# Optimization experiments

Measured on AMD Instinct MI355X. Metric: run time of the kernel, lower is better.

The kernel has to match this reference:

```python
import jax, jax.numpy as jnp
import numpy as np

N = 50000
E = 800000
IN_CH = 128
HID = 16
HEADS = 8
OUT_CH = 64
NEG_SLOPE = 0.2


def setup_inputs() -> dict:
    key = jax.random.key(0)
    ks = jax.random.split(key, 16)
    x = jax.random.normal(ks[0], (N, IN_CH), dtype=jnp.float32)
    edge_index = jax.random.randint(ks[1], (2, E), 0, N, dtype=jnp.int64)
    s = 0.05
    # GATv2 layer 1: in=128 -> heads=8, out=16 (concat -> 128)
    W1l = jax.random.normal(ks[2], (IN_CH, HEADS * HID), dtype=jnp.float32) * s
    b1l = jnp.zeros((HEADS * HID,), dtype=jnp.float32)
    W1r = jax.random.normal(ks[3], (IN_CH, HEADS * HID), dtype=jnp.float32) * s
    b1r = jnp.zeros((HEADS * HID,), dtype=jnp.float32)
    att1 = jax.random.normal(ks[4], (HEADS, HID), dtype=jnp.float32) * s
    bias1 = jnp.zeros((HEADS * HID,), dtype=jnp.float32)
    # GATv2 layer 2: in=128 -> heads=1, out=64
    W2l = jax.random.normal(ks[5], (HEADS * HID, OUT_CH), dtype=jnp.float32) * s
    b2l = jnp.zeros((OUT_CH,), dtype=jnp.float32)
    W2r = jax.random.normal(ks[6], (HEADS * HID, OUT_CH), dtype=jnp.float32) * s
    b2r = jnp.zeros((OUT_CH,), dtype=jnp.float32)
    att2 = jax.random.normal(ks[7], (1, OUT_CH), dtype=jnp.float32) * s
    bias2 = jnp.zeros((OUT_CH,), dtype=jnp.float32)
    return dict(x=x, edge_index=edge_index,
                W1l=W1l, b1l=b1l, W1r=W1r, b1r=b1r, att1=att1, bias1=bias1,
                W2l=W2l, b2l=b2l, W2r=W2r, b2r=b2r, att2=att2, bias2=bias2)


def gatv2_conv(x, src, dst, Wl, bl, Wr, br, att, bias, heads, out_ch, concat):
    n = x.shape[0]
    xl = (x @ Wl + bl).reshape(n, heads, out_ch)  # source transform
    xr = (x @ Wr + br).reshape(n, heads, out_ch)  # target transform
    m = xl[src] + xr[dst]                          # [E, H, C]
    m = jnp.where(m > 0, m, NEG_SLOPE * m)         # LeakyReLU(0.2)
    alpha = jnp.einsum('ehc,hc->eh', m, att)       # [E, H]
    # segment softmax over destination nodes (every node has a self loop)
    amax = jax.ops.segment_max(alpha, dst, num_segments=n)
    ea = jnp.exp(alpha - amax[dst])
    denom = jax.ops.segment_sum(ea, dst, num_segments=n)
    w = ea / denom[dst]                            # [E, H]
    out = jax.ops.segment_sum(xl[src] * w[:, :, None], dst, num_segments=n)
    if concat:
        out = out.reshape(n, heads * out_ch)
    else:
        out = out.mean(axis=1)
    return out + bias


def reference(x, edge_index, W1l, b1l, W1r, b1r, att1, bias1,
              W2l, b2l, W2r, b2r, att2, bias2):
    n = x.shape[0]
    loops = jnp.arange(n, dtype=edge_index.dtype)
    src = jnp.concatenate([edge_index[0], loops])
    dst = jnp.concatenate([edge_index[1], loops])
    # dropout layers are identity in eval mode
    h = gatv2_conv(x, src, dst, W1l, b1l, W1r, b1r, att1, bias1,
                   heads=HEADS, out_ch=HID, concat=True)
    h = jax.nn.elu(h)
    out = gatv2_conv(h, src, dst, W2l, b2l, W2r, b2r, att2, bias2,
                     heads=1, out_ch=OUT_CH, concat=True)
    return out
```

## Files before the change

### kernel.cpp

```cpp
#include <hip/hip_runtime.h>
#include <hip/hip_bf16.h>

constexpr int N_  = 50000;
constexpr int E_  = 800000;
constexpr int ET_ = 850000;
constexpr float NEG_SLOPE = 0.2f;

constexpr int CAP  = 48;
constexpr int HT   = ET_ / 8;
constexpr int SB   = (HT + 255) / 256;
constexpr int G1B  = N_ / 16;
constexpr int ZERO4 = (N_ * CAP + N_) / 4;

typedef __attribute__((ext_vector_type(8))) short short8;
typedef __attribute__((ext_vector_type(4))) float f32x4;

__device__ inline unsigned bf16rn(float f) {
    union { float f; unsigned u; } v; v.f = f;
    return (v.u + 0x7fffu + ((v.u >> 16) & 1u)) >> 16;
}
__device__ inline float2 unpack2(unsigned u) {
    return make_float2(__uint_as_float(u << 16), __uint_as_float(u & 0xffff0000u));
}

__global__ __launch_bounds__(256) void init_kernel(
        const float* __restrict__ W1l, const float* __restrict__ W1r,
        const float* __restrict__ W2l, const float* __restrict__ W2r,
        unsigned short* __restrict__ wsw, unsigned short* __restrict__ wsw2,
        int4* __restrict__ zbase) {
    int gid = blockIdx.x * 256 + threadIdx.x;
    if (gid < ZERO4) zbase[gid] = make_int4(0, 0, 0, 0);
    if (gid < 32768) {
        int j    = gid & 7;
        int lane = (gid >> 3) & 63;
        int ks   = (gid >> 9) & 3;
        int ct   = gid >> 11;
        int k = ks * 32 + ((lane >> 4) & 3) * 8 + j;
        int c = ct * 16 + (lane & 15);
        float v = (c < 128) ? W1l[k * 128 + c] : W1r[k * 128 + (c - 128)];
        wsw[gid] = (unsigned short)bf16rn(v);
    } else if (gid < 49152) {
        int t2   = gid - 32768;
        int j    = t2 & 7;
        int lane = (t2 >> 3) & 63;
        int ks   = (t2 >> 9) & 3;
        int ct   = t2 >> 11;
        int k = ks * 32 + ((lane >> 4) & 3) * 8 + j;
        int c = ct * 16 + (lane & 15);
        float v = (c < 64) ? W2l[k * 64 + c] : W2r[k * 64 + (c - 64)];
        wsw2[t2] = (unsigned short)bf16rn(v);
    }
}

__global__ __launch_bounds__(256) void scatter_gemm1(
        const int* __restrict__ ei, int* __restrict__ cur,
        int* __restrict__ csr_src,
        const float* __restrict__ x, const unsigned short* __restrict__ wsw,
        const float* __restrict__ bl, const float* __restrict__ br,
        const float* __restrict__ att1,
        unsigned short* __restrict__ xlu, float* __restrict__ xr1,
        float* __restrict__ A1) {
    __shared__ unsigned short lu[16][132];
    __shared__ float          lr[16][132];
    if (blockIdx.x < SB) {
        int t = blockIdx.x * 256 + threadIdx.x;
        if (t >= HT) return;
        int e8 = t * 8;
        int s[8], d[8];
        if (e8 < E_) {
            int4 sa = *(const int4*)(ei + e8);
            int4 sb = *(const int4*)(ei + e8 + 4);
            int4 da = *(const int4*)(ei + E_ + e8);
            int4 db = *(const int4*)(ei + E_ + e8 + 4);
            s[0] = sa.x; s[1] = sa.y; s[2] = sa.z; s[3] = sa.w;
            s[4] = sb.x; s[5] = sb.y; s[6] = sb.z; s[7] = sb.w;
            d[0] = da.x; d[1] = da.y; d[2] = da.z; d[3] = da.w;
            d[4] = db.x; d[5] = db.y; d[6] = db.z; d[7] = db.w;
        } else {
            #pragma unroll
            for (int i = 0; i < 8; ++i) { s[i] = e8 + i - E_; d[i] = s[i]; }
        }
        int o[8];
        #pragma unroll
        for (int i = 0; i < 8; ++i) o[i] = atomicAdd(&cur[d[i]], 1);
        #pragma unroll
        for (int i = 0; i < 8; ++i)
            if (o[i] < CAP) csr_src[d[i] * CAP + o[i]] = s[i];
        return;
    }
    const int blk  = blockIdx.x - SB;
    const int wave = threadIdx.x >> 6;
    const int lane = threadIdx.x & 63;
    const int n0 = blk * 16;
    const int m = lane & 15;
    const int q = (lane >> 4) & 3;
    const float* __restrict__ arow = x + (size_t)(n0 + m) * 128 + q * 8;
    short8 afrag[4];
    #pragma unroll
    for (int ks = 0; ks < 4; ++ks) {
        float4 v0 = *(const float4*)(arow + ks * 32);
        float4 v1 = *(const float4*)(arow + ks * 32 + 4);
        short8 a;
        a[0] = (short)bf16rn(v0.x); a[1] = (short)bf16rn(v0.y);
        a[2] = (short)bf16rn(v0.z); a[3] = (short)bf16rn(v0.w);
        a[4] = (short)bf16rn(v1.x); a[5] = (short)bf16rn(v1.y);
        a[6] = (short)bf16rn(v1.z); a[7] = (short)bf16rn(v1.w);
        afrag[ks] = a;
    }
    #pragma unroll
    for (int i = 0; i < 4; ++i) {
        const int ct = wave * 4 + i;
        f32x4 acc = {0.f, 0.f, 0.f, 0.f};
        #pragma unroll
        for (int ks = 0; ks < 4; ++ks) {
            short8 b = *(const short8*)(wsw + ((size_t)(ct * 4 + ks) * 64 + lane) * 8);
            acc = __builtin_amdgcn_mfma_f32_16x16x32_bf16(afrag[ks], b, acc, 0, 0, 0);
        }
        if (ct < 8) {
            const int col = ct * 16 + m;
            float bias = bl[col];
            #pragma unroll
            for (int j = 0; j < 4; ++j)
                lu[q * 4 + j][col] = (unsigned short)bf16rn(acc[j] + bias);
        } else {
            const int col = (ct - 8) * 16 + m;
            float bias = br[col];
            #pragma unroll
            for (int j = 0; j < 4; ++j)
                lr[q * 4 + j][col] = acc[j] + bias;
        }
    }
    __syncthreads();
    unsigned* __restrict__ xlu32 = (unsigned*)xlu;
    #pragma unroll
    for (int k = 0; k < 4; ++k) {
        int r = wave * 4 + k;
        unsigned w = *(const unsigned*)&lu[r][2 * lane];
        xlu32[(size_t)(n0 + r) * 64 + lane] = w;
        float2 f = make_float2(lr[r][2 * lane], lr[r][2 * lane + 1]);
        *(float2*)(xr1 + (size_t)(n0 + r) * 128 + 2 * lane) = f;
    }
    {
        const int h = lane >> 3;
        const int i = lane & 7;
        float2 avh = *(const float2*)(att1 + h * 16 + 2 * i);
        avh.x *= 0.6f; avh.y *= 0.6f;
        #pragma unroll
        for (int k = 0; k < 4; ++k) {
            int r = wave * 4 + k;
            float2 v = unpack2(*(const unsigned*)&lu[r][h * 16 + 2 * i]);
            float p = fmaf(v.x, avh.x, v.y * avh.y);
            p += __shfl_xor(p, 1);
            p += __shfl_xor(p, 2);
            p += __shfl_xor(p, 4);
            if (i == 0) A1[(size_t)(n0 + r) * 8 + h] = p;
        }
    }
}

__global__ __launch_bounds__(256) void fused1(
        const int* __restrict__ csr_src, const int* __restrict__ cnt,
        const unsigned* __restrict__ xl1b, const float* __restrict__ xr1,
        const float* __restrict__ att, const float* __restrict__ bias1,
        const float* __restrict__ A1, float* __restrict__ hout) {
    int t = blockIdx.x * 256 + threadIdx.x;
    int n = __builtin_amdgcn_readfirstlane(t >> 6);
    int lane = t & 63;
    if (n >= N_) return;
    const int half = lane >> 5;
    const int li   = lane & 31;
    const int h    = li >> 2;
    float4 xr = *(const float4*)(xr1 + (size_t)n * 128 + 4 * li);
    float4 av = *(const float4*)(att + 4 * li);
    av.x *= 0.4f; av.y *= 0.4f; av.z *= 0.4f; av.w *= 0.4f;
    int p0 = n * CAP;
    int c  = __builtin_amdgcn_readfirstlane(cnt[n]);
    if (c > CAP) c = CAP;
    int p1 = p0 + c;
    float4 acc = {0.f, 0.f, 0.f, 0.f};
    float l = 0.f;
    for (int p = p0; p < p1; p += 8) {
        #pragma unroll
        for (int u = 0; u < 4; ++u) {
            int pe = p + 2 * u + half;
            int s  = csr_src[pe];
            float g = A1[(size_t)s * 8 + h];
            uint2 xw = *(const uint2*)(xl1b + (size_t)s * 64 + 2 * li);
            float2 v01 = unpack2(xw.x);
            float2 v23 = unpack2(xw.y);
            float a = fmaf(fabsf(v01.y + xr.y), av.y, fabsf(v01.x + xr.x) * av.x);
            a = fmaf(fabsf(v23.x + xr.z), av.z, a);
            a = fmaf(fabsf(v23.y + xr.w), av.w, a);
            a += __shfl_xor(a, 1);
            a += __shfl_xor(a, 2);
            float w = pe < p1 ? __expf(a + g) : 0.f;
            acc.x = fmaf(w, v01.x, acc.x);
            acc.y = fmaf(w, v01.y, acc.y);
            acc.z = fmaf(w, v23.x, acc.z);
            acc.w = fmaf(w, v23.y, acc.w);
            l += w;
        }
    }
    acc.x += __shfl_xor(acc.x, 32);
    acc.y += __shfl_xor(acc.y, 32);
    acc.z += __shfl_xor(acc.z, 32);
    acc.w += __shfl_xor(acc.w, 32);
    l     += __shfl_xor(l, 32);
    if (half == 0) {
        float4 bv = *(const float4*)(bias1 + 4 * li);
        float4 o;
        float vx;
        vx = acc.x / l + bv.x; o.x = vx > 0.f ? vx : (__expf(vx) - 1.f);
        vx = acc.y / l + bv.y; o.y = vx > 0.f ? vx : (__expf(vx) - 1.f);
        vx = acc.z / l + bv.z; o.z = vx > 0.f ? vx : (__expf(vx) - 1.f);
        vx = acc.w / l + bv.w; o.w = vx > 0.f ? vx : (__expf(vx) - 1.f);
        *(float4*)(hout + (size_t)n * 128 + 4 * li) = o;
    }
}

__global__ __launch_bounds__(256) void gemm2_mfma(
        const float* __restrict__ hbuf,
        const unsigned short* __restrict__ wsw2,
        const float* __restrict__ bl, const float* __restrict__ br,
        const float* __restrict__ att2,
        unsigned short* __restrict__ xlu2, float* __restrict__ xr2,
        float* __restrict__ A2) {
    __shared__ unsigned short lu2[16][68];
    __shared__ float          lr2[16][68];
    const int wave = threadIdx.x >> 6;
    const int lane = threadIdx.x & 63;
    const int n0 = blockIdx.x * 16;
    const int m = lane & 15;
    const int q = (lane >> 4) & 3;
    const float* __restrict__ arow = hbuf + (size_t)(n0 + m) * 128 + q * 8;
    short8 afrag[4];
    #pragma unroll
    for (int ks = 0; ks < 4; ++ks) {
        float4 v0 = *(const float4*)(arow + ks * 32);
        float4 v1 = *(const float4*)(arow + ks * 32 + 4);
        short8 a;
        a[0] = (short)bf16rn(v0.x); a[1] = (short)bf16rn(v0.y);
        a[2] = (short)bf16rn(v0.z); a[3] = (short)bf16rn(v0.w);
        a[4] = (short)bf16rn(v1.x); a[5] = (short)bf16rn(v1.y);
        a[6] = (short)bf16rn(v1.z); a[7] = (short)bf16rn(v1.w);
        afrag[ks] = a;
    }
    #pragma unroll
    for (int i = 0; i < 2; ++i) {
        const int ct = wave * 2 + i;
        f32x4 acc = {0.f, 0.f, 0.f, 0.f};
        #pragma unroll
        for (int ks = 0; ks < 4; ++ks) {
            short8 b = *(const short8*)(wsw2 + ((size_t)(ct * 4 + ks) * 64 + lane) * 8);
            acc = __builtin_amdgcn_mfma_f32_16x16x32_bf16(afrag[ks], b, acc, 0, 0, 0);
        }
        if (ct < 4) {
            const int col = ct * 16 + m;
            float bias = bl[col];
            #pragma unroll
            for (int j = 0; j < 4; ++j)
                lu2[q * 4 + j][col] = (unsigned short)bf16rn(acc[j] + bias);
        } else {
            const int col = (ct - 4) * 16 + m;
            float bias = br[col];
            #pragma unroll
            for (int j = 0; j < 4; ++j)
                lr2[q * 4 + j][col] = acc[j] + bias;
        }
    }
    __syncthreads();
    unsigned* __restrict__ xlu232 = (unsigned*)xlu2;
    #pragma unroll
    for (int k = 0; k < 2; ++k) {
        int rr = wave * 4 + 2 * k + (lane >> 5);
        int cc = lane & 31;
        unsigned w = *(const unsigned*)&lu2[rr][2 * cc];
        xlu232[(size_t)(n0 + rr) * 32 + cc] = w;
    }
    #pragma unroll
    for (int k = 0; k < 4; ++k) {
        int r = wave * 4 + k;
        xr2[(size_t)(n0 + r) * 64 + lane] = lr2[r][lane];
    }
    {
        const int i2 = lane & 31;
        float2 av2 = *(const float2*)(att2 + 2 * i2);
        av2.x *= 0.6f; av2.y *= 0.6f;
        #pragma unroll
        for (int k = 0; k < 4; ++k) {
            int r = wave * 4 + k;
            float2 v = unpack2(*(const unsigned*)&lu2[r][2 * i2]);
            float p = fmaf(v.x, av2.x, v.y * av2.y);
            p += __shfl_xor(p, 1);
            p += __shfl_xor(p, 2);
            p += __shfl_xor(p, 4);
            p += __shfl_xor(p, 8);
            p += __shfl_xor(p, 16);
            if (lane == 0) A2[n0 + r] = p;
        }
    }
}

__global__ __launch_bounds__(256) void fused2(
        const int* __restrict__ csr_src, const int* __restrict__ cnt,
        const unsigned* __restrict__ xl2b, const float* __restrict__ xr2,
        const float* __restrict__ att, const float* __restrict__ bias2,
        const float* __restrict__ A2, float* __restrict__ out) {
    int t = blockIdx.x * 256 + threadIdx.x;
    int n = __builtin_amdgcn_readfirstlane(t >> 6);
    int lane = t & 63;
    if (n >= N_) return;
    const int g4 = lane >> 4;
    const int li = lane & 15;
    float4 xr = *(const float4*)(xr2 + (size_t)n * 64 + 4 * li);
    float4 av = *(const float4*)(att + 4 * li);
    av.x *= 0.4f; av.y *= 0.4f; av.z *= 0.4f; av.w *= 0.4f;
    int p0 = n * CAP;
    int c  = __builtin_amdgcn_readfirstlane(cnt[n]);
    if (c > CAP) c = CAP;
    int p1 = p0 + c;
    float4 acc = {0.f, 0.f, 0.f, 0.f};
    float l = 0.f;
    for (int p = p0; p < p1; p += 8) {
        #pragma unroll
        for (int u = 0; u < 2; ++u) {
            int pe = p + 4 * u + g4;
            int s  = csr_src[pe];
            float g = A2[s];
            uint2 xw = *(const uint2*)(xl2b + (size_t)s * 32 + 2 * li);
            float2 v01 = unpack2(xw.x);
            float2 v23 = unpack2(xw.y);
            float a = fmaf(fabsf(v01.y + xr.y), av.y, fabsf(v01.x + xr.x) * av.x);
            a = fmaf(fabsf(v23.x + xr.z), av.z, a);
            a = fmaf(fabsf(v23.y + xr.w), av.w, a);
            a += __shfl_xor(a, 1);
            a += __shfl_xor(a, 2);
            a += __shfl_xor(a, 4);
            a += __shfl_xor(a, 8);
            float w = pe < p1 ? __expf(a + g) : 0.f;
            acc.x = fmaf(w, v01.x, acc.x);
            acc.y = fmaf(w, v01.y, acc.y);
            acc.z = fmaf(w, v23.x, acc.z);
            acc.w = fmaf(w, v23.y, acc.w);
            l += w;
        }
    }
    acc.x += __shfl_xor(acc.x, 16); acc.y += __shfl_xor(acc.y, 16);
    acc.z += __shfl_xor(acc.z, 16); acc.w += __shfl_xor(acc.w, 16);
    l     += __shfl_xor(l, 16);
    acc.x += __shfl_xor(acc.x, 32); acc.y += __shfl_xor(acc.y, 32);
    acc.z += __shfl_xor(acc.z, 32); acc.w += __shfl_xor(acc.w, 32);
    l     += __shfl_xor(l, 32);
    if (lane < 16) {
        float4 bv = *(const float4*)(bias2 + 4 * li);
        float4 o;
        o.x = acc.x / l + bv.x;
        o.y = acc.y / l + bv.y;
        o.z = acc.z / l + bv.z;
        o.w = acc.w / l + bv.w;
        *(float4*)(out + (size_t)n * 64 + 4 * li) = o;
    }
}

extern "C" void kernel_launch(void* const* d_in, const int* in_sizes, int n_in,
                              void* d_out, int out_size, void* d_ws, size_t ws_size,
                              hipStream_t stream) {
    (void)in_sizes; (void)n_in; (void)out_size; (void)ws_size;
    const float* x     = (const float*)d_in[0];
    const int*   ei    = (const int*)d_in[1];
    const float* W1l   = (const float*)d_in[2];
    const float* b1l   = (const float*)d_in[3];
    const float* W1r   = (const float*)d_in[4];
    const float* b1r   = (const float*)d_in[5];
    const float* att1  = (const float*)d_in[6];
    const float* bias1 = (const float*)d_in[7];
    const float* W2l   = (const float*)d_in[8];
    const float* b2l   = (const float*)d_in[9];
    const float* W2r   = (const float*)d_in[10];
    const float* b2r   = (const float*)d_in[11];
    const float* att2  = (const float*)d_in[12];
    const float* bias2 = (const float*)d_in[13];
    float* out = (float*)d_out;

    float* xr1      = (float*)d_ws;
    float* hbuf     = xr1 + 6400000;
    unsigned* xl1b  = (unsigned*)(hbuf + 6400000);
    int* csr_src = (int*)(xl1b + 3200000);
    int* cur     = csr_src + 2400000;
    float* A1    = (float*)(cur + 50000);
    unsigned short* wsw2 = (unsigned short*)(A1 + 400000);
    float* A2      = A1;
    unsigned* xl2b = xl1b;
    float* xr2     = xr1;
    unsigned short* wsw = (unsigned short*)hbuf;

    init_kernel<<<(ZERO4 + 255) / 256, 256, 0, stream>>>(W1l, W1r, W2l, W2r,
                                                         wsw, wsw2, (int4*)csr_src);
    scatter_gemm1<<<SB + G1B, 256, 0, stream>>>(ei, cur, csr_src, x, wsw,
                                                b1l, b1r, att1,
                                                (unsigned short*)xl1b, xr1, A1);
    fused1<<<(N_ * 64 + 255) / 256, 256, 0, stream>>>(csr_src, cur, xl1b, xr1,
                                                      att1, bias1, A1, hbuf);
    gemm2_mfma<<<N_ / 16, 256, 0, stream>>>(hbuf, wsw2, b2l, b2r, att2,
                                            (unsigned short*)xl2b, xr2, A2);
    fused2<<<(N_ * 64 + 255) / 256, 256, 0, stream>>>(csr_src, cur, xl2b, xr2,
                                                      att2, bias2, A2, out);
}
```

Baseline: 247.9 us.

## Fuse layer-1 aggregation with layer-2 MFMA projection via shared memory

Merges the layer-1 edge aggregation kernel and the layer-2 GEMM into one 512-thread kernel. Each block aggregates 16 nodes into a shared-memory tile of h, then runs the bf16 MFMA projection from that tile. This removes the global write and re-read of the 50000x128 fp32 hidden buffer and one kernel launch. Layer-2 outputs are moved to a separate workspace region because the layer-1 buffers they used to overwrite are still being read. The cost is a larger block with a barrier, where each wave handles two nodes serially, which may reduce latency hiding in the gather loop.

```diff
diff --git a/kernel.cpp b/kernel.cpp
--- a/kernel.cpp
+++ b/kernel.cpp
@@ -10,6 +10,7 @@
 constexpr int HT   = ET_ / 8;
 constexpr int SB   = (HT + 255) / 256;
 constexpr int G1B  = N_ / 16;
+constexpr int FB   = N_ / 16;
 constexpr int ZERO4 = (N_ * CAP + N_) / 4;
 
 typedef __attribute__((ext_vector_type(8))) short short8;
@@ -158,96 +159,94 @@
     }
 }
 
-__global__ __launch_bounds__(256) void fused1(
+__global__ __launch_bounds__(512) void fused1g2(
         const int* __restrict__ csr_src, const int* __restrict__ cnt,
         const unsigned* __restrict__ xl1b, const float* __restrict__ xr1,
         const float* __restrict__ att, const float* __restrict__ bias1,
-        const float* __restrict__ A1, float* __restrict__ hout) {
-    int t = blockIdx.x * 256 + threadIdx.x;
-    int n = __builtin_amdgcn_readfirstlane(t >> 6);
-    int lane = t & 63;
-    if (n >= N_) return;
+        const float* __restrict__ A1,
+        const unsigned short* __restrict__ wsw2,
+        const float* __restrict__ b2l, const float* __restrict__ b2r,
+        const float* __restrict__ att2,
+        unsigned short* __restrict__ xlu2, float* __restrict__ xr2,
+        float* __restrict__ A2) {
+    __shared__ float          hsh[16][132];
+    __shared__ unsigned short lu2[16][68];
+    __shared__ float          lr2[16][68];
+    const int wv   = threadIdx.x >> 6;
+    const int lane = threadIdx.x & 63;
+    const int n0   = blockIdx.x * 16;
     const int half = lane >> 5;
     const int li   = lane & 31;
     const int h    = li >> 2;
-    float4 xr = *(const float4*)(xr1 + (size_t)n * 128 + 4 * li);
+
     float4 av = *(const float4*)(att + 4 * li);
     av.x *= 0.4f; av.y *= 0.4f; av.z *= 0.4f; av.w *= 0.4f;
-    int p0 = n * CAP;
-    int c  = __builtin_amdgcn_readfirstlane(cnt[n]);
-    if (c > CAP) c = CAP;
-    int p1 = p0 + c;
-    float4 acc = {0.f, 0.f, 0.f, 0.f};
-    float l = 0.f;
-    for (int p = p0; p < p1; p += 8) {
-        #pragma unroll
-        for (int u = 0; u < 4; ++u) {
-            int pe = p + 2 * u + half;
-            int s  = csr_src[pe];
-            float g = A1[(size_t)s * 8 + h];
-            uint2 xw = *(const uint2*)(xl1b + (size_t)s * 64 + 2 * li);
-            float2 v01 = unpack2(xw.x);
-            float2 v23 = unpack2(xw.y);
-            float a = fmaf(fabsf(v01.y + xr.y), av.y, fabsf(v01.x + xr.x) * av.x);
-            a = fmaf(fabsf(v23.x + xr.z), av.z, a);
-            a = fmaf(fabsf(v23.y + xr.w), av.w, a);
-            a += __shfl_xor(a, 1);
-            a += __shfl_xor(a, 2);
-            float w = pe < p1 ? __expf(a + g) : 0.f;
-            acc.x = fmaf(w, v01.x, acc.x);
-            acc.y = fmaf(w, v01.y, acc.y);
-            acc.z = fmaf(w, v23.x, acc.z);
-            acc.w = fmaf(w, v23.y, acc.w);
-            l += w;
-        }
-    }
-    acc.x += __shfl_xor(acc.x, 32);
-    acc.y += __shfl_xor(acc.y, 32);
-    acc.z += __shfl_xor(acc.z, 32);
-    acc.w += __shfl_xor(acc.w, 32);
-    l     += __shfl_xor(l, 32);
-    if (half == 0) {
-        float4 bv = *(const float4*)(bias1 + 4 * li);
-        float4 o;
-        float vx;
-        vx = acc.x / l + bv.x; o.x = vx > 0.f ? vx : (__expf(vx) - 1.f);
-        vx = acc.y / l + bv.y; o.y = vx > 0.f ? vx : (__expf(vx) - 1.f);
-        vx = acc.z / l + bv.z; o.z = vx > 0.f ? vx : (__expf(vx) - 1.f);
-        vx = acc.w / l + bv.w; o.w = vx > 0.f ? vx : (__expf(vx) - 1.f);
-        *(float4*)(hout + (size_t)n * 128 + 4 * li) = o;
-    }
-}
-
-__global__ __launch_bounds__(256) void gemm2_mfma(
-        const float* __restrict__ hbuf,
-        const unsigned short* __restrict__ wsw2,
-        const float* __restrict__ bl, const float* __restrict__ br,
-        const float* __restrict__ att2,
-        unsigned short* __restrict__ xlu2, float* __restrict__ xr2,
-        float* __restrict__ A2) {
-    __shared__ unsigned short lu2[16][68];
-    __shared__ float          lr2[16][68];
-    const int wave = threadIdx.x >> 6;
-    const int lane = threadIdx.x & 63;
-    const int n0 = blockIdx.x * 16;
-    const int m = lane & 15;
-    const int q = (lane >> 4) & 3;
-    const float* __restrict__ arow = hbuf + (size_t)(n0 + m) * 128 + q * 8;
-    short8 afrag[4];
     #pragma unroll
-    for (int ks = 0; ks < 4; ++ks) {
-        float4 v0 = *(const float4*)(arow + ks * 32);
-        float4 v1 = *(const float4*)(arow + ks * 32 + 4);
-        short8 a;
-        a[0] = (short)bf16rn(v0.x); a[1] = (short)bf16rn(v0.y);
-        a[2] = (short)bf16rn(v0.z); a[3] = (short)bf16rn(v0.w);
-        a[4] = (short)bf16rn(v1.x); a[5] = (short)bf16rn(v1.y);
-        a[6] = (short)bf16rn(v1.z); a[7] = (short)bf16rn(v1.w);
-        afrag[ks] = a;
-    }
-    #pragma unroll
-    for (int i = 0; i < 2; ++i) {
-        const int ct = wave * 2 + i;
+    for (int j = 0; j < 2; ++j) {
+        const int n = __builtin_amdgcn_readfirstlane(n0 + 2 * wv + j);
+        float4 xr = *(const float4*)(xr1 + (size_t)n * 128 + 4 * li);
+        int p0 = n * CAP;
+        int c  = __builtin_amdgcn_readfirstlane(cnt[n]);
+        if (c > CAP) c = CAP;
+        int p1 = p0 + c;
+        float4 acc = {0.f, 0.f, 0.f, 0.f};
+        float l = 0.f;
+        for (int p = p0; p < p1; p += 8) {
+            #pragma unroll
+            for (int u = 0; u < 4; ++u) {
+                int pe = p + 2 * u + half;
+                int s  = csr_src[pe];
+                float g = A1[(size_t)s * 8 + h];
+                uint2 xw = *(const uint2*)(xl1b + (size_t)s * 64 + 2 * li);
+                float2 v01 = unpack2(xw.x);
+                float2 v23 = unpack2(xw.y);
+                float a = fmaf(fabsf(v01.y + xr.y), av.y, fabsf(v01.x + xr.x) * av.x);
+                a = fmaf(fabsf(v23.x + xr.z), av.z, a);
+                a = fmaf(fabsf(v23.y + xr.w), av.w, a);
+                a += __shfl_xor(a, 1);
+                a += __shfl_xor(a, 2);
+                float w = pe < p1 ? __expf(a + g) : 0.f;
+                acc.x = fmaf(w, v01.x, acc.x);
+                acc.y = fmaf(w, v01.y, acc.y);
+                acc.z = fmaf(w, v23.x, acc.z);
+                acc.w = fmaf(w, v23.y, acc.w);
+                l += w;
+            }
+        }
+        acc.x += __shfl_xor(acc.x, 32);
+        acc.y += __shfl_xor(acc.y, 32);
+        acc.z += __shfl_xor(acc.z, 32);
+        acc.w += __shfl_xor(acc.w, 32);
+        l     += __shfl_xor(l, 32);
+        if (half == 0) {
+            float4 bv = *(const float4*)(bias1 + 4 * li);
+            float4 o;
+            float vx;
+            vx = acc.x / l + bv.x; o.x = vx > 0.f ? vx : (__expf(vx) - 1.f);
+            vx = acc.y / l + bv.y; o.y = vx > 0.f ? vx : (__expf(vx) - 1.f);
+            vx = acc.z / l + bv.z; o.z = vx > 0.f ? vx : (__expf(vx) - 1.f);
+            vx = acc.w / l + bv.w; o.w = vx > 0.f ? vx : (__expf(vx) - 1.f);
+            *(float4*)(&hsh[2 * wv + j][4 * li]) = o;
+        }
+    }
+    __syncthreads();
+
+    {
+        const int m = lane & 15;
+        const int q = (lane >> 4) & 3;
+        short8 afrag[4];
+        #pragma unroll
+        for (int ks = 0; ks < 4; ++ks) {
+            float4 v0 = *(const float4*)(&hsh[m][q * 8 + ks * 32]);
+            float4 v1 = *(const float4*)(&hsh[m][q * 8 + ks * 32 + 4]);
+            short8 a;
+            a[0] = (short)bf16rn(v0.x); a[1] = (short)bf16rn(v0.y);
+            a[2] = (short)bf16rn(v0.z); a[3] = (short)bf16rn(v0.w);
+            a[4] = (short)bf16rn(v1.x); a[5] = (short)bf16rn(v1.y);
+            a[6] = (short)bf16rn(v1.z); a[7] = (short)bf16rn(v1.w);
+            afrag[ks] = a;
+        }
+        const int ct = wv;
         f32x4 acc = {0.f, 0.f, 0.f, 0.f};
         #pragma unroll
         for (int ks = 0; ks < 4; ++ks) {
@@ -256,39 +255,34 @@
         }
         if (ct < 4) {
             const int col = ct * 16 + m;
-            float bias = bl[col];
+            float bias = b2l[col];
             #pragma unroll
             for (int j = 0; j < 4; ++j)
                 lu2[q * 4 + j][col] = (unsigned short)bf16rn(acc[j] + bias);
         } else {
             const int col = (ct - 4) * 16 + m;
-            float bias = br[col];
+            float bias = b2r[col];
             #pragma unroll
             for (int j = 0; j < 4; ++j)
                 lr2[q * 4 + j][col] = acc[j] + bias;
         }
     }
     __syncthreads();
-    unsigned* __restrict__ xlu232 = (unsigned*)xlu2;
-    #pragma unroll
-    for (int k = 0; k < 2; ++k) {
-        int rr = wave * 4 + 2 * k + (lane >> 5);
-        int cc = lane & 31;
-        unsigned w = *(const unsigned*)&lu2[rr][2 * cc];
-        xlu232[(size_t)(n0 + rr) * 32 + cc] = w;
-    }
-    #pragma unroll
-    for (int k = 0; k < 4; ++k) {
-        int r = wave * 4 + k;
-        xr2[(size_t)(n0 + r) * 64 + lane] = lr2[r][lane];
-    }
     {
+        const int row = threadIdx.x >> 5;
+        const int c   = threadIdx.x & 31;
+        unsigned w = *(const unsigned*)&lu2[row][2 * c];
+        ((unsigned*)xlu2)[(size_t)(n0 + row) * 32 + c] = w;
+        float2 f = make_float2(lr2[row][2 * c], lr2[row][2 * c + 1]);
+        *(float2*)(xr2 + (size_t)(n0 + row) * 64 + 2 * c) = f;
+    }
+    if (wv < 4) {
         const int i2 = lane & 31;
         float2 av2 = *(const float2*)(att2 + 2 * i2);
         av2.x *= 0.6f; av2.y *= 0.6f;
         #pragma unroll
         for (int k = 0; k < 4; ++k) {
-            int r = wave * 4 + k;
+            int r = wv * 4 + k;
             float2 v = unpack2(*(const unsigned*)&lu2[r][2 * i2]);
             float p = fmaf(v.x, av2.x, v.y * av2.y);
             p += __shfl_xor(p, 1);
@@ -383,26 +377,25 @@
     float* out = (float*)d_out;
 
     float* xr1      = (float*)d_ws;
-    float* hbuf     = xr1 + 6400000;
-    unsigned* xl1b  = (unsigned*)(hbuf + 6400000);
+    float* hregion  = xr1 + 6400000;
+    unsigned* xl1b  = (unsigned*)(hregion + 6400000);
     int* csr_src = (int*)(xl1b + 3200000);
     int* cur     = csr_src + 2400000;
     float* A1    = (float*)(cur + 50000);
     unsigned short* wsw2 = (unsigned short*)(A1 + 400000);
-    float* A2      = A1;
-    unsigned* xl2b = xl1b;
-    float* xr2     = xr1;
-    unsigned short* wsw = (unsigned short*)hbuf;
+    unsigned short* wsw = (unsigned short*)hregion;
+    unsigned* xl2b = (unsigned*)(hregion + 16384);
+    float* xr2     = hregion + 16384 + 1600000;
+    float* A2      = hregion + 16384 + 1600000 + 3200000;
 
     init_kernel<<<(ZERO4 + 255) / 256, 256, 0, stream>>>(W1l, W1r, W2l, W2r,
                                                          wsw, wsw2, (int4*)csr_src);
     scatter_gemm1<<<SB + G1B, 256, 0, stream>>>(ei, cur, csr_src, x, wsw,
                                                 b1l, b1r, att1,
                                                 (unsigned short*)xl1b, xr1, A1);
-    fused1<<<(N_ * 64 + 255) / 256, 256, 0, stream>>>(csr_src, cur, xl1b, xr1,
-                                                      att1, bias1, A1, hbuf);
-    gemm2_mfma<<<N_ / 16, 256, 0, stream>>>(hbuf, wsw2, b2l, b2r, att2,
-                                            (unsigned short*)xl2b, xr2, A2);
+    fused1g2<<<FB, 512, 0, stream>>>(csr_src, cur, xl1b, xr1, att1, bias1, A1,
+                                     wsw2, b2l, b2r, att2,
+                                     (unsigned short*)xl2b, xr2, A2);
     fused2<<<(N_ * 64 + 255) / 256, 256, 0, stream>>>(csr_src, cur, xl2b, xr2,
                                                       att2, bias2, A2, out);
 }
```

Measured after the change: 254.9 us. 2.8% more time.
